# Optimization experiments

Measured on AMD Instinct MI355X. Metric: run time of the kernel, lower is better.

The kernel has to match this reference:

```python
import jax, jax.numpy as jnp
import numpy as np

TAU = 0.07
EPS_NORM = 1e-12
EPS_DEN = 1e-8


def setup_inputs() -> dict:
    key = jax.random.key(0)
    k1, k2, k3, k4 = jax.random.split(key, 4)
    B, C, H, W = 2, 128, 64, 64
    return {
        "input": jax.random.normal(k1, (B, C, H, W), dtype=jnp.float32),
        "target": jax.random.normal(k2, (B, C, H, W), dtype=jnp.float32),
        "input_seg": jax.random.randint(k3, (B, H, W), 0, 4, dtype=jnp.int64 if jax.config.jax_enable_x64 else jnp.int32),
        "target_seg": jax.random.randint(k4, (B, H, W), 0, 4, dtype=jnp.int64 if jax.config.jax_enable_x64 else jnp.int32),
    }


def _flatten_normalize(x):
    # (B, C, H, W) -> (B*H*W, C), L2-normalized rows (torch F.normalize semantics)
    B, C = x.shape[0], x.shape[1]
    x = jnp.moveaxis(x, 1, -1).reshape(-1, C)
    norm = jnp.linalg.norm(x, axis=-1, keepdims=True)
    return x / jnp.maximum(norm, EPS_NORM)


def reference(input, target, input_seg, target_seg):
    ni = _flatten_normalize(input)    # (N, C)
    nt = _flatten_normalize(target)   # (N, C)
    pi = input_seg.reshape(-1)        # (N,)
    pt = target_seg.reshape(-1)       # (N,)

    # sim[a, b] = cos(target[a], input[b]); rows already unit-norm so dot == cosine
    sim = jnp.einsum("ac,bc->ab", nt, ni)
    sim_exp = jnp.exp(sim / TAU)

    # diff[a, b] = 1 if pred_input[b] != pred_target[a]
    diff = (pi[None, :] != pt[:, None]).astype(jnp.float32)

    nominator = jnp.sum((1.0 - diff) * sim_exp, axis=0)          # (N,) positives per input pixel
    denominator = jnp.sum(diff * sim_exp, axis=0) + nominator    # (N,) all pairs
    loss = -jnp.log(nominator / (denominator + EPS_DEN)).mean()
    return loss
```

## Files before the change

### kernel.cpp

```cpp
#include <hip/hip_runtime.h>

#define N_PIX 8192
#define C_DIM 128
#define TAU_INV_LOG2E 20.609929155556622f
#define EPS_DEN 1e-8f
#define NT_TILES 68
#define NT_ROWS (NT_TILES * 128)
#define FAKE_ROWS (NT_ROWS - N_PIX)

typedef unsigned short u16;
typedef __attribute__((ext_vector_type(8))) short short8;
typedef __attribute__((ext_vector_type(4))) float f32x4;

__device__ __forceinline__ u16 f2bf(float f) {
    unsigned u = __float_as_uint(f);
    return (u16)((u + 0x7fffu + ((u >> 16) & 1u)) >> 16);
}

struct P1 {
    float tile[128][33];
    float sscale[32];
    int sdest[32];
    int chunkcnt[256][4];
    int pfx[256][4];
    int tot[4];
};
struct P2 { u16 sA[128 * 128]; };
struct P3 { float part[4]; };
union SMem { P1 p1; P2 p2; P3 p3; };


__device__ __forceinline__ void phase1(SMem& sm, int bid, int t,
                                       const float* __restrict__ input,
                                       const float* __restrict__ target,
                                       const int* __restrict__ tseg,
                                       int* __restrict__ meta,
                                       u16* __restrict__ ni_bf,
                                       u16* __restrict__ nt_sorted,
                                       float* __restrict__ den,
                                       float* __restrict__ nom) {
    int lane = t & 63, w = t >> 6;
    int arr = bid >> 8;
    int u = bid & 255;
    int bb = u >> 7;
    int hw0 = (u & 127) * 32;
    const float* src = (arr ? target : input) + bb * (C_DIM * 4096);

    if (arr == 0) {
        if (t < 32) den[u * 32 + t] = 0.f;
        else if (t < 64) nom[u * 32 + (t - 32)] = 0.f;
        if (bid == 0 && t >= 64 && t < 73) meta[t - 64] = 0;
    }

    int c8 = t >> 5, hwl = t & 31;
#pragma unroll
    for (int i = 0; i < 16; ++i) {
        int c = i * 8 + c8;
        sm.p1.tile[c][hwl] = src[c * 4096 + hw0 + hwl];
    }

    int ps[5] = {0, 0, 0, 0, 0};
    int padc[4] = {0, 0, 0, 0};
    if (arr) {
        int c0 = 0, c1 = 0, c2 = 0, c3 = 0;
        const int4* ts4 = (const int4*)tseg;
#pragma unroll
        for (int j = 0; j < 8; ++j) {
            int4 x = ts4[t * 8 + j];
            c0 += (x.x == 0) + (x.y == 0) + (x.z == 0) + (x.w == 0);
            c1 += (x.x == 1) + (x.y == 1) + (x.z == 1) + (x.w == 1);
            c2 += (x.x == 2) + (x.y == 2) + (x.z == 2) + (x.w == 2);
            c3 += (x.x == 3) + (x.y == 3) + (x.z == 3) + (x.w == 3);
        }
        sm.p1.chunkcnt[t][0] = c0; sm.p1.chunkcnt[t][1] = c1;
        sm.p1.chunkcnt[t][2] = c2; sm.p1.chunkcnt[t][3] = c3;
    }
    __syncthreads();

    if (arr) {
        int c = w;
        int vv[4];
#pragma unroll
        for (int j = 0; j < 4; ++j) vv[j] = sm.p1.chunkcnt[lane * 4 + j][c];
        int s = vv[0] + vv[1] + vv[2] + vv[3];
        int si = s;
#pragma unroll
        for (int off = 1; off < 64; off <<= 1) {
            int y = __shfl_up(si, off);
            if (lane >= off) si += y;
        }
        int run = si - s;
#pragma unroll
        for (int j = 0; j < 4; ++j) { sm.p1.pfx[lane * 4 + j][c] = run; run += vv[j]; }
        if (lane == 63) sm.p1.tot[c] = si;
    }
    __syncthreads();

    if (arr) {
#pragma unroll
        for (int c = 0; c < 4; ++c) {
            int tc = sm.p1.tot[c];
            int padded = (tc + 127) & ~127;
            ps[c + 1] = ps[c] + padded;
            padc[c] = padded - tc;
        }
        if (u == 0) {
            if (t < 4) meta[12 + t] = padc[t];
            if (t < NT_TILES) {
                int row = t * 128, cl = 4;
#pragma unroll
                for (int c = 0; c < 4; ++c)
                    if (row >= ps[c] && row < ps[c + 1]) cl = c;
                meta[16 + t] = cl;
            }
        }
        if (t < 32) {
            int g = u * 2 + (t >> 4);
            int gg = g, c;
            for (c = 0; c < 4; ++c) { if (gg < padc[c]) break; gg -= padc[c]; }
            int row = (c < 4) ? (ps[c + 1] - padc[c] + gg) : (ps[4] + gg);
            short8 z = {};
            *(short8*)(nt_sorted + (long)row * C_DIM + (t & 15) * 8) = z;
        }
    }

    int p = t >> 3, sub = t & 7;
    float ss = 0.f;
#pragma unroll
    for (int i = 0; i < 16; ++i) {
        float vv = sm.p1.tile[sub * 16 + i][p];
        ss += vv * vv;
    }
    ss += __shfl_xor(ss, 1);
    ss += __shfl_xor(ss, 2);
    ss += __shfl_xor(ss, 4);
    if (sub == 0) {
        float sc = 1.0f / fmaxf(sqrtf(ss), 1e-12f);
        int n = bb * 4096 + hw0 + p;
        int dst_row;
        if (arr) {
            sc *= TAU_INV_LOG2E;
            int cme = tseg[n];
            const int* tc32 = tseg + (n & ~31);
            int r = 0;
            for (int j = 0; j < p; ++j) r += (tc32[j] == cme);
            dst_row = ps[cme] + sm.p1.pfx[n >> 5][cme] + r;
        } else {
            dst_row = n;
        }
        sm.p1.sscale[p] = sc;
        sm.p1.sdest[p] = dst_row;
    }
    __syncthreads();

    u16* dst = arr ? nt_sorted : ni_bf;
#pragma unroll
    for (int i = 0; i < 2; ++i) {
        int idx = t + i * 256;
        int px = idx >> 4, kc = idx & 15;
        float sc = sm.p1.sscale[px];
        long drow = sm.p1.sdest[px];
        short8 o;
#pragma unroll
        for (int j = 0; j < 8; ++j)
            o[j] = (short)f2bf(sm.p1.tile[kc * 8 + j][px] * sc);
        *(short8*)(dst + drow * C_DIM + kc * 8) = o;
    }
}

__device__ __forceinline__ void phase2(SMem& sm, int bid, int t,
                                       const u16* __restrict__ ni,
                                       const u16* __restrict__ nt,
                                       const int* __restrict__ piseg,
                                       const int* __restrict__ meta,
                                       float* __restrict__ den,
                                       float* __restrict__ nom) {
    int lane = t & 63, w = t >> 6;
    int bcb = bid & 63;
    int as  = bid >> 6;
    int t0  = as * 8 + (as < 4 ? as : 4);
    int ntl = 8 + (as < 4 ? 1 : 0);
    int bcol0 = bcb * 128;
    int wr = w >> 1, wc = w & 1;
    int l15 = lane & 15, q = lane >> 4;
    const int* tcls = meta + 16;

    short8 bfrag[4][4];
    int pil[4];
#pragma unroll
    for (int ct = 0; ct < 4; ++ct) {
        int brow = bcol0 + wc * 64 + ct * 16 + l15;
        pil[ct] = piseg[brow];
        const u16* bp = ni + brow * C_DIM + q * 8;
#pragma unroll
        for (int kc = 0; kc < 4; ++kc)
            bfrag[ct][kc] = *(const short8*)(bp + kc * 32);
    }

    float den_l[4] = {0.f, 0.f, 0.f, 0.f};
    float nom_l[4] = {0.f, 0.f, 0.f, 0.f};

    for (int it = 0; it < ntl; ++it) {
        int tile = t0 + it;
        int a0 = tile * 128;
        __syncthreads();
        {
            const uint4* gsrc = (const uint4*)(nt + (long)a0 * C_DIM);
#pragma unroll
            for (int i = 0; i < 8; ++i) {
                int idx = t + i * 256;
                int r = idx >> 4, ch = idx & 15;
                int sw = ch ^ (r & 15);
                *(uint4*)(&sm.p2.sA[r * 128 + sw * 8]) = gsrc[idx];
            }
        }
        __syncthreads();

        f32x4 acc[4][4] = {};
#pragma unroll
        for (int kc = 0; kc < 4; ++kc) {
            short8 af[4];
#pragma unroll
            for (int rt = 0; rt < 4; ++rt) {
                int ar = wr * 64 + rt * 16 + l15;
                int sw = (kc * 4 + q) ^ l15;
                af[rt] = *(const short8*)(&sm.p2.sA[ar * 128 + sw * 8]);
            }
#pragma unroll
            for (int rt = 0; rt < 4; ++rt)
#pragma unroll
                for (int ct = 0; ct < 4; ++ct)
                    acc[rt][ct] = __builtin_amdgcn_mfma_f32_16x16x32_bf16(
                        af[rt], bfrag[ct][kc], acc[rt][ct], 0, 0, 0);
        }

        int tc = tcls[tile];
        float td[4] = {0.f, 0.f, 0.f, 0.f};
#pragma unroll
        for (int rt = 0; rt < 4; ++rt)
#pragma unroll
            for (int ct = 0; ct < 4; ++ct) {
                f32x4 v = acc[rt][ct];
                float e0 = __builtin_amdgcn_exp2f(v[0]);
                float e1 = __builtin_amdgcn_exp2f(v[1]);
                float e2 = __builtin_amdgcn_exp2f(v[2]);
                float e3 = __builtin_amdgcn_exp2f(v[3]);
                td[ct] += (e0 + e1) + (e2 + e3);
            }
#pragma unroll
        for (int ct = 0; ct < 4; ++ct) {
            den_l[ct] += td[ct];
            nom_l[ct] += (tc == pil[ct]) ? td[ct] : 0.f;
        }
    }

#pragma unroll
    for (int ct = 0; ct < 4; ++ct) {
        float d = den_l[ct], nm = nom_l[ct];
        d += __shfl_xor(d, 16); d += __shfl_xor(d, 32);
        nm += __shfl_xor(nm, 16); nm += __shfl_xor(nm, 32);
        if (lane < 16) {
            int b = bcol0 + wc * 64 + ct * 16 + lane;
            atomicAdd(&den[b], d);
            atomicAdd(&nom[b], nm);
        }
    }
}

__device__ __forceinline__ void phase3(SMem& sm, int t,
                                       const float* __restrict__ den,
                                       const float* __restrict__ nom,
                                       const int* __restrict__ piseg,
                                       const int* __restrict__ meta,
                                       float* __restrict__ out) {
    float padcf[4];
#pragma unroll
    for (int c = 0; c < 4; ++c) padcf[c] = (float)meta[12 + c];
    int base = t * 32;
    float s = 0.f;
#pragma unroll
    for (int h = 0; h < 4; ++h) {
        float dv[8], nv[8];
        int pc[8];
#pragma unroll
        for (int j = 0; j < 8; ++j) {
            int i = base + h * 8 + j;
            dv[j] = __hip_atomic_load(den + i, __ATOMIC_RELAXED, __HIP_MEMORY_SCOPE_AGENT);
            nv[j] = __hip_atomic_load(nom + i, __ATOMIC_RELAXED, __HIP_MEMORY_SCOPE_AGENT);
            pc[j] = piseg[i];
        }
#pragma unroll
        for (int j = 0; j < 8; ++j) {
            float nm = nv[j] - padcf[pc[j]];
            float dd = dv[j] - (float)FAKE_ROWS;
            s -= __logf(nm / (dd + EPS_DEN));
        }
    }
#pragma unroll
    for (int off = 32; off > 0; off >>= 1) s += __shfl_down(s, off);
    if ((t & 63) == 0) sm.p3.part[t >> 6] = s;
    __syncthreads();
    if (t == 0)
        out[0] = (sm.p3.part[0] + sm.p3.part[1] + sm.p3.part[2] + sm.p3.part[3])
                 * (1.0f / N_PIX);
}

__global__ __launch_bounds__(256) void p1_k(const float* __restrict__ input,
                                            const float* __restrict__ target,
                                            const int* __restrict__ tseg,
                                            int* __restrict__ meta,
                                            u16* __restrict__ ni_bf,
                                            u16* __restrict__ nt_sorted,
                                            float* __restrict__ den,
                                            float* __restrict__ nom) {
    __shared__ __align__(16) SMem sm;
    phase1(sm, blockIdx.x, threadIdx.x, input, target, tseg, meta, ni_bf, nt_sorted, den, nom);
}

__global__ __launch_bounds__(256, 2) void main_loss_k(const u16* __restrict__ ni,
                                                      const u16* __restrict__ nt,
                                                      const int* __restrict__ piseg,
                                                      int* __restrict__ meta,
                                                      float* __restrict__ den,
                                                      float* __restrict__ nom,
                                                      float* __restrict__ out) {
    __shared__ __align__(16) SMem sm;
    __shared__ int is_last;
    int t = threadIdx.x;
    phase2(sm, blockIdx.x, t, ni, nt, piseg, meta, den, nom);
    __syncthreads();
    if (t == 0) {
        int leaf = blockIdx.x >> 6;
        int lk = atomicAdd(&meta[leaf], 1);
        int last = 0;
        if (lk == 63) {
            int rk = atomicAdd(&meta[8], 1);
            last = (rk == 7);
        }
        is_last = last;
    }
    __syncthreads();
    if (is_last) phase3(sm, t, den, nom, piseg, meta, out);
}

extern "C" void kernel_launch(void* const* d_in, const int* in_sizes, int n_in,
                              void* d_out, int out_size, void* d_ws, size_t ws_size,
                              hipStream_t stream) {
    const float* input  = (const float*)d_in[0];
    const float* target = (const float*)d_in[1];
    const int*   iseg   = (const int*)d_in[2];
    const int*   tseg   = (const int*)d_in[3];
    float* out = (float*)d_out;

    char* ws = (char*)d_ws;
    u16* ni_bf     = (u16*)(ws);
    u16* nt_sorted = (u16*)(ws + 0x200000);
    float* den     = (float*)(ws + 0x420000);
    float* nom     = (float*)(ws + 0x428000);
    int* meta      = (int*)(ws + 0x430000);

    p1_k<<<512, 256, 0, stream>>>(input, target, tseg, meta, ni_bf, nt_sorted, den, nom);
    main_loss_k<<<512, 256, 0, stream>>>(ni_bf, nt_sorted, iseg, meta, den, nom, out);
}
```

Baseline: 105.6 us.

## Load A fragments directly from global memory instead of staging through LDS

The main similarity kernel no longer cooperatively copies each 128-row tile of normalized target rows into swizzled shared memory with two barriers per tile. Each wave now loads its A-operand MFMA fragments straight from global (L2-cached) memory into registers. This removes the per-tile barriers and LDS traffic and frees shared memory, which may allow more blocks to be resident. In exchange, the two waves that share a row half each load the same A data redundantly from global memory, and the extra register pressure for 16 fragments may reduce occupancy.

Result: slower. 121.5 us (+15.1%).

```diff
diff --git a/kernel.cpp b/kernel.cpp
--- a/kernel.cpp
+++ b/kernel.cpp
@@ -25,12 +25,9 @@
     int pfx[256][4];
     int tot[4];
 };
-struct P2 { u16 sA[128 * 128]; };
-struct P3 { float part[4]; };
-union SMem { P1 p1; P2 p2; P3 p3; };
-
-
-__device__ __forceinline__ void phase1(SMem& sm, int bid, int t,
+
+
+__device__ __forceinline__ void phase1(P1& sm, int bid, int t,
                                        const float* __restrict__ input,
                                        const float* __restrict__ target,
                                        const int* __restrict__ tseg,
@@ -56,7 +53,7 @@
 #pragma unroll
     for (int i = 0; i < 16; ++i) {
         int c = i * 8 + c8;
-        sm.p1.tile[c][hwl] = src[c * 4096 + hw0 + hwl];
+        sm.tile[c][hwl] = src[c * 4096 + hw0 + hwl];
     }
 
     int ps[5] = {0, 0, 0, 0, 0};
@@ -72,8 +69,8 @@
             c2 += (x.x == 2) + (x.y == 2) + (x.z == 2) + (x.w == 2);
             c3 += (x.x == 3) + (x.y == 3) + (x.z == 3) + (x.w == 3);
         }
-        sm.p1.chunkcnt[t][0] = c0; sm.p1.chunkcnt[t][1] = c1;
-        sm.p1.chunkcnt[t][2] = c2; sm.p1.chunkcnt[t][3] = c3;
+        sm.chunkcnt[t][0] = c0; sm.chunkcnt[t][1] = c1;
+        sm.chunkcnt[t][2] = c2; sm.chunkcnt[t][3] = c3;
     }
     __syncthreads();
 
@@ -81,7 +78,7 @@
         int c = w;
         int vv[4];
 #pragma unroll
-        for (int j = 0; j < 4; ++j) vv[j] = sm.p1.chunkcnt[lane * 4 + j][c];
+        for (int j = 0; j < 4; ++j) vv[j] = sm.chunkcnt[lane * 4 + j][c];
         int s = vv[0] + vv[1] + vv[2] + vv[3];
         int si = s;
 #pragma unroll
@@ -91,15 +88,15 @@
         }
         int run = si - s;
 #pragma unroll
-        for (int j = 0; j < 4; ++j) { sm.p1.pfx[lane * 4 + j][c] = run; run += vv[j]; }
-        if (lane == 63) sm.p1.tot[c] = si;
+        for (int j = 0; j < 4; ++j) { sm.pfx[lane * 4 + j][c] = run; run += vv[j]; }
+        if (lane == 63) sm.tot[c] = si;
     }
     __syncthreads();
 
     if (arr) {
 #pragma unroll
         for (int c = 0; c < 4; ++c) {
-            int tc = sm.p1.tot[c];
+            int tc = sm.tot[c];
             int padded = (tc + 127) & ~127;
             ps[c + 1] = ps[c] + padded;
             padc[c] = padded - tc;
@@ -128,7 +125,7 @@
     float ss = 0.f;
 #pragma unroll
     for (int i = 0; i < 16; ++i) {
-        float vv = sm.p1.tile[sub * 16 + i][p];
+        float vv = sm.tile[sub * 16 + i][p];
         ss += vv * vv;
     }
     ss += __shfl_xor(ss, 1);
@@ -144,12 +141,12 @@
             const int* tc32 = tseg + (n & ~31);
             int r = 0;
             for (int j = 0; j < p; ++j) r += (tc32[j] == cme);
-            dst_row = ps[cme] + sm.p1.pfx[n >> 5][cme] + r;
+            dst_row = ps[cme] + sm.pfx[n >> 5][cme] + r;
         } else {
             dst_row = n;
         }
-        sm.p1.sscale[p] = sc;
-        sm.p1.sdest[p] = dst_row;
+        sm.sscale[p] = sc;
+        sm.sdest[p] = dst_row;
     }
     __syncthreads();
 
@@ -158,17 +155,17 @@
     for (int i = 0; i < 2; ++i) {
         int idx = t + i * 256;
         int px = idx >> 4, kc = idx & 15;
-        float sc = sm.p1.sscale[px];
-        long drow = sm.p1.sdest[px];
+        float sc = sm.sscale[px];
+        long drow = sm.sdest[px];
         short8 o;
 #pragma unroll
         for (int j = 0; j < 8; ++j)
-            o[j] = (short)f2bf(sm.p1.tile[kc * 8 + j][px] * sc);
+            o[j] = (short)f2bf(sm.tile[kc * 8 + j][px] * sc);
         *(short8*)(dst + drow * C_DIM + kc * 8) = o;
     }
 }
 
-__device__ __forceinline__ void phase2(SMem& sm, int bid, int t,
+__device__ __forceinline__ void phase2(int bid, int t,
                                        const u16* __restrict__ ni,
                                        const u16* __restrict__ nt,
                                        const int* __restrict__ piseg,
@@ -200,39 +197,28 @@
     float den_l[4] = {0.f, 0.f, 0.f, 0.f};
     float nom_l[4] = {0.f, 0.f, 0.f, 0.f};
 
+    const u16* abase = nt + (long)(t0 * 128 + wr * 64 + l15) * C_DIM + q * 8;
+
     for (int it = 0; it < ntl; ++it) {
         int tile = t0 + it;
-        int a0 = tile * 128;
-        __syncthreads();
-        {
-            const uint4* gsrc = (const uint4*)(nt + (long)a0 * C_DIM);
-#pragma unroll
-            for (int i = 0; i < 8; ++i) {
-                int idx = t + i * 256;
-                int r = idx >> 4, ch = idx & 15;
-                int sw = ch ^ (r & 15);
-                *(uint4*)(&sm.p2.sA[r * 128 + sw * 8]) = gsrc[idx];
-            }
-        }
-        __syncthreads();
+        const u16* ap = abase + (long)it * 128 * C_DIM;
+
+        short8 af[4][4];
+#pragma unroll
+        for (int rt = 0; rt < 4; ++rt)
+#pragma unroll
+            for (int kc = 0; kc < 4; ++kc)
+                af[rt][kc] = *(const short8*)(ap + rt * 16 * C_DIM + kc * 32);
 
         f32x4 acc[4][4] = {};
 #pragma unroll
-        for (int kc = 0; kc < 4; ++kc) {
-            short8 af[4];
-#pragma unroll
-            for (int rt = 0; rt < 4; ++rt) {
-                int ar = wr * 64 + rt * 16 + l15;
-                int sw = (kc * 4 + q) ^ l15;
-                af[rt] = *(const short8*)(&sm.p2.sA[ar * 128 + sw * 8]);
-            }
+        for (int kc = 0; kc < 4; ++kc)
 #pragma unroll
             for (int rt = 0; rt < 4; ++rt)
 #pragma unroll
                 for (int ct = 0; ct < 4; ++ct)
                     acc[rt][ct] = __builtin_amdgcn_mfma_f32_16x16x32_bf16(
-                        af[rt], bfrag[ct][kc], acc[rt][ct], 0, 0, 0);
-        }
+                        af[rt][kc], bfrag[ct][kc], acc[rt][ct], 0, 0, 0);
 
         int tc = tcls[tile];
         float td[4] = {0.f, 0.f, 0.f, 0.f};
@@ -267,7 +253,7 @@
     }
 }
 
-__device__ __forceinline__ void phase3(SMem& sm, int t,
+__device__ __forceinline__ void phase3(float* __restrict__ part, int t,
                                        const float* __restrict__ den,
                                        const float* __restrict__ nom,
                                        const int* __restrict__ piseg,
@@ -298,11 +284,10 @@
     }
 #pragma unroll
     for (int off = 32; off > 0; off >>= 1) s += __shfl_down(s, off);
-    if ((t & 63) == 0) sm.p3.part[t >> 6] = s;
+    if ((t & 63) == 0) part[t >> 6] = s;
     __syncthreads();
     if (t == 0)
-        out[0] = (sm.p3.part[0] + sm.p3.part[1] + sm.p3.part[2] + sm.p3.part[3])
-                 * (1.0f / N_PIX);
+        out[0] = (part[0] + part[1] + part[2] + part[3]) * (1.0f / N_PIX);
 }
 
 __global__ __launch_bounds__(256) void p1_k(const float* __restrict__ input,
@@ -313,7 +298,7 @@
                                             u16* __restrict__ nt_sorted,
                                             float* __restrict__ den,
                                             float* __restrict__ nom) {
-    __shared__ __align__(16) SMem sm;
+    __shared__ __align__(16) P1 sm;
     phase1(sm, blockIdx.x, threadIdx.x, input, target, tseg, meta, ni_bf, nt_sorted, den, nom);
 }
 
@@ -324,10 +309,10 @@
                                                       float* __restrict__ den,
                                                       float* __restrict__ nom,
                                                       float* __restrict__ out) {
-    __shared__ __align__(16) SMem sm;
+    __shared__ float part[4];
     __shared__ int is_last;
     int t = threadIdx.x;
-    phase2(sm, blockIdx.x, t, ni, nt, piseg, meta, den, nom);
+    phase2(blockIdx.x, t, ni, nt, piseg, meta, den, nom);
     __syncthreads();
     if (t == 0) {
         int leaf = blockIdx.x >> 6;
@@ -340,7 +325,7 @@
         is_last = last;
     }
     __syncthreads();
-    if (is_last) phase3(sm, t, den, nom, piseg, meta, out);
+    if (is_last) phase3(part, t, den, nom, piseg, meta, out);
 }
 
 extern "C" void kernel_launch(void* const* d_in, const int* in_sizes, int n_in,
```
